# Kernel optimization log

Measured on AMD Instinct MI355X. Metric: run time of the kernel, lower is better.

Reference implementation:

```python
import jax, jax.numpy as jnp
import numpy as np

B, N, D, H = 4, 4096, 1024, 16
HD = D // H  # head dim = 64


def setup_inputs() -> dict:
    key = jax.random.key(0)
    k1, k2, k3 = jax.random.split(key, 3)
    x = jax.random.normal(k1, (B, N, D), dtype=jnp.float32)
    Wqkv = jax.random.normal(k2, (3 * D, D), dtype=jnp.float32) * (1.0 / np.sqrt(D))
    Wo = jax.random.normal(k3, (D, D), dtype=jnp.float32) * (1.0 / np.sqrt(D))
    bo = jnp.zeros((D,), dtype=jnp.float32)
    return {"x": x, "Wqkv": Wqkv, "Wo": Wo, "bo": bo}


def reference(x, Wqkv, Wo, bo):
    # qkv projection (no bias): [B,N,3D] -> [B,N,3,H,HD]
    qkv = jnp.einsum('bnd,ed->bne', x, Wqkv).reshape(B, N, 3, H, HD)
    q, k, v = qkv[:, :, 0], qkv[:, :, 1], qkv[:, :, 2]  # each [B,N,H,HD]
    # NOTE: faithful to source — heads are NOT moved to a batch axis, so
    # scores are [B,N,H,H]: attention mixes across heads per token.
    scores = jnp.einsum('bnhd,bngd->bnhg', q, k) / jnp.sqrt(jnp.float32(D))
    w = jax.nn.softmax(scores, axis=-1)            # [B,N,H,H]
    attn = jnp.einsum('bnhg,bngd->bnhd', w, v)     # [B,N,H,HD]
    attn = attn.reshape(B, N, D)
    return jnp.einsum('bnd,ed->bne', attn, Wo) + bo
```

## Files before the change

### kernel.cpp

```cpp
#include <hip/hip_runtime.h>
#include <hip/hip_bf16.h>

using bf16 = __hip_bfloat16;
typedef __attribute__((ext_vector_type(8))) short bf16x8;
typedef __attribute__((ext_vector_type(4))) float f32x4;

#define GLL(gp, lp) __builtin_amdgcn_global_load_lds( \
    (const __attribute__((address_space(1))) void*)(gp), \
    (__attribute__((address_space(3))) void*)(lp), 16, 0, 0)

#define BAR()    asm volatile("s_barrier" ::: "memory")
#define WAITV4() asm volatile("s_waitcnt vmcnt(4)" ::: "memory")
#define WAITV6() asm volatile("s_waitcnt vmcnt(6)" ::: "memory")
#define WAITV0() asm volatile("s_waitcnt vmcnt(0)" ::: "memory")
#define WAITL0() do { asm volatile("s_waitcnt lgkmcnt(0)" ::: "memory"); \
                      __builtin_amdgcn_sched_barrier(0); } while (0)
#define LHINT8() asm volatile("s_waitcnt lgkmcnt(8)" ::: "memory")

__device__ inline short bfbits(float f) {
  union { bf16 h; short s; } u;
  u.h = __float2bfloat16(f);
  return u.s;
}

__device__ inline bf16x8 ldcvt(const float* __restrict__ g) {
  const float4 f0 = *(const float4*)(g);
  const float4 f1 = *(const float4*)(g + 4);
  union { short s[8]; bf16x8 v; } u;
  u.s[0] = bfbits(f0.x); u.s[1] = bfbits(f0.y); u.s[2] = bfbits(f0.z); u.s[3] = bfbits(f0.w);
  u.s[4] = bfbits(f1.x); u.s[5] = bfbits(f1.y); u.s[6] = bfbits(f1.z); u.s[7] = bfbits(f1.w);
  return u.v;
}

__global__ __launch_bounds__(256)
void f32_to_bf16(const float* __restrict__ src, bf16* __restrict__ dst, int n8) {
  const int i = blockIdx.x * 256 + threadIdx.x;
  if (i < n8) *(bf16x8*)(dst + (size_t)i * 8) = ldcvt(src + (size_t)i * 8);
}

template <typename TC, bool SPLIT3>
__global__ __launch_bounds__(512)
void gemm256(const bf16* __restrict__ A, const bf16* __restrict__ B,
             const float* __restrict__ bias, TC* __restrict__ C,
             int K, int lda, int ldb, int ldc, int nbx) {
  __shared__ __align__(16) bf16 smem[4][256][64];
  const int tid  = threadIdx.x;
  const int lane = tid & 63;
  const int wave = tid >> 6;
  const int wm = wave >> 2;
  const int wn = wave & 3;

  int wg = blockIdx.x;
  const int nwg = gridDim.x;
  if ((nwg & 7) == 0) wg = (wg & 7) * (nwg >> 3) + (wg >> 3);
  const int m0 = (wg / nbx) * 256;
  const int n0 = (wg % nbx) * 256;

  const int srow = wave * 8 + (lane >> 3);
  const int scol = ((lane & 7) ^ (lane >> 3)) * 8;
  const bf16* gA = A + (size_t)(m0 + srow) * lda + scol;
  const bf16* gB = B + (size_t)(n0 + srow) * ldb + scol;

  const int fr = lane & 15, quad = lane >> 4, swz = fr & 7;

#define STAGE_A(buf, h, kt) do { \
    GLL(gA + (size_t)((h) * 128     ) * lda + (kt) * 64, &smem[buf][(h) * 128      + wave * 8][0]); \
    GLL(gA + (size_t)((h) * 128 + 64) * lda + (kt) * 64, &smem[buf][(h) * 128 + 64 + wave * 8][0]); \
  } while (0)
#define STAGE_B(buf, h, kt) do { \
    GLL(gB + (size_t)((h) * 128     ) * ldb + (kt) * 64, &smem[2 + (buf)][(h) * 128      + wave * 8][0]); \
    GLL(gB + (size_t)((h) * 128 + 64) * ldb + (kt) * 64, &smem[2 + (buf)][(h) * 128 + 64 + wave * 8][0]); \
  } while (0)
#define LDA_G(buf, mh) do { _Pragma("unroll") \
    for (int t = 0; t < 4; ++t) { _Pragma("unroll") \
      for (int ks = 0; ks < 2; ++ks) \
        av[t * 2 + ks] = *(const bf16x8*)&smem[buf][wm * 128 + (mh) * 64 + t * 16 + fr] \
                                             [(((ks << 2) | quad) ^ swz) << 3]; } } while (0)
#define LDB_G(buf, nh, dst) do { _Pragma("unroll") \
    for (int t = 0; t < 2; ++t) { _Pragma("unroll") \
      for (int ks = 0; ks < 2; ++ks) \
        dst[t * 2 + ks] = *(const bf16x8*)&smem[2 + (buf)][wn * 64 + (nh) * 32 + t * 16 + fr] \
                                              [(((ks << 2) | quad) ^ swz) << 3]; } } while (0)
#define MFMA_Q(mh, nh, bb) do { \
    __builtin_amdgcn_s_setprio(1); \
    _Pragma("unroll") \
    for (int t = 0; t < 4; ++t) { _Pragma("unroll") \
      for (int u = 0; u < 2; ++u) { _Pragma("unroll") \
        for (int ks = 0; ks < 2; ++ks) \
          acc[(mh) * 4 + t][(nh) * 2 + u] = __builtin_amdgcn_mfma_f32_16x16x32_bf16( \
              av[t * 2 + ks], bb[u * 2 + ks], acc[(mh) * 4 + t][(nh) * 2 + u], 0, 0, 0); } } \
    __builtin_amdgcn_s_setprio(0); } while (0)

  bf16x8 av[8], b0[4], b1[4];
  f32x4 acc[8][4] = {};

  STAGE_A(0, 0, 0); STAGE_A(0, 1, 0);
  STAGE_B(0, 0, 0); STAGE_B(0, 1, 0);
  STAGE_B(1, 0, 1); STAGE_B(1, 1, 1);
  STAGE_A(1, 0, 1);
  WAITV6(); BAR();

  const int KT = K >> 6;
  const int NI = KT >> 1;
  for (int i = 0; i < NI; ++i) {
    const int kt1 = 2 * i + 1;
    const int ka  = (2 * i + 2 < KT) ? 2 * i + 2 : 0;
    const int kb  = (2 * i + 3 < KT) ? 2 * i + 3 : 0;

    LDA_G(0, 0); LDB_G(0, 0, b0); STAGE_A(1, 1, kt1);
    LHINT8();
    BAR(); WAITL0(); MFMA_Q(0, 0, b0); BAR();
    LDB_G(0, 1, b1);
    BAR(); WAITL0(); MFMA_Q(0, 1, b1); BAR();
    LDA_G(0, 1); STAGE_B(0, 0, ka);
    BAR(); WAITL0(); MFMA_Q(1, 1, b1); BAR();
    STAGE_B(0, 1, ka); WAITV4();
    BAR(); WAITL0(); MFMA_Q(1, 0, b0); BAR();
    LDA_G(1, 0); LDB_G(1, 0, b0); STAGE_A(0, 0, ka);
    LHINT8();
    BAR(); WAITL0(); MFMA_Q(0, 0, b0); BAR();
    LDB_G(1, 1, b1); STAGE_A(0, 1, ka);
    BAR(); WAITL0(); MFMA_Q(0, 1, b1); BAR();
    LDA_G(1, 1); STAGE_B(1, 0, kb);
    BAR(); WAITL0(); MFMA_Q(1, 1, b1); BAR();
    STAGE_B(1, 1, kb); STAGE_A(1, 0, kb); WAITV6();
    BAR(); WAITL0(); MFMA_Q(1, 0, b0); BAR();
  }
  WAITV0(); BAR();

  const int rq = quad * 4;
  char* myc = (char*)(&smem[0][0][0]) + wave * 16384;
  float bvv[4];
#pragma unroll
  for (int nj = 0; nj < 4; ++nj)
    bvv[nj] = bias ? bias[n0 + wn * 64 + nj * 16 + fr] : 0.0f;

  const int cn0 = n0 + wn * 64;

  if constexpr (sizeof(TC) == 2) {
#pragma unroll
    for (int mi = 0; mi < 8; ++mi)
#pragma unroll
      for (int nj = 0; nj < 4; ++nj)
#pragma unroll
        for (int r = 0; r < 4; ++r) {
          const int row   = mi * 16 + rq + r;
          const int chunk = ((nj << 1) | (fr >> 3)) ^ (row & 7);
          *(short*)(myc + row * 128 + chunk * 16 + (fr & 7) * 2) =
              bfbits(acc[mi][nj][r] + bvv[nj]);
        }
    asm volatile("s_waitcnt lgkmcnt(0)" ::: "memory");
    __builtin_amdgcn_sched_barrier(0);
    const int rr = lane >> 3, rc = (lane & 7) ^ (lane >> 3);
    size_t cbase;
    if constexpr (SPLIT3)
      cbase = ((size_t)(cn0 >> 10) << 24) + (size_t)(m0 + wm * 128) * 1024 + (cn0 & 1023);
    else
      cbase = (size_t)(m0 + wm * 128) * ldc + cn0;
    const int cstride = SPLIT3 ? 1024 : ldc;
#pragma unroll
    for (int j = 0; j < 16; ++j) {
      const int row = j * 8 + rr;
      const uint4 d = *(const uint4*)(myc + row * 128 + rc * 16);
      *(uint4*)((bf16*)C + cbase + (size_t)row * cstride + (lane & 7) * 8) = d;
    }
  } else {
#pragma unroll
    for (int p = 0; p < 2; ++p) {
#pragma unroll
      for (int mi = 0; mi < 4; ++mi)
#pragma unroll
        for (int nj = 0; nj < 4; ++nj)
#pragma unroll
          for (int r = 0; r < 4; ++r) {
            const int row   = mi * 16 + rq + r;
            const int col   = nj * 16 + fr;
            const int chunk = (col >> 2) ^ (row & 7);
            *(float*)(myc + row * 256 + chunk * 16 + (col & 3) * 4) =
                acc[p * 4 + mi][nj][r] + bvv[nj];
          }
      asm volatile("s_waitcnt lgkmcnt(0)" ::: "memory");
      __builtin_amdgcn_sched_barrier(0);
      const int rr = lane >> 4, rc0 = lane & 15;
#pragma unroll
      for (int j = 0; j < 16; ++j) {
        const int row   = j * 4 + rr;
        const int chunk = rc0 ^ (row & 7);
        const uint4 d = *(const uint4*)(myc + row * 256 + chunk * 16);
        *(uint4*)((float*)C + (size_t)(m0 + wm * 128 + p * 64 + row) * ldc
                  + cn0 + rc0 * 4) = d;
      }
      if (p == 0) {
        asm volatile("s_waitcnt lgkmcnt(0)" ::: "memory");
        __builtin_amdgcn_sched_barrier(0);
      }
    }
  }
#undef STAGE_A
#undef STAGE_B
#undef LDA_G
#undef LDB_G
#undef MFMA_Q
}

__global__ __launch_bounds__(256)
void attn_heads(bf16* __restrict__ qp, const bf16* __restrict__ kp,
                const bf16* __restrict__ vp) {
  __shared__ __align__(16) bf16  s_qkv[4][3072];
  __shared__ __align__(16) float s_w[4][256];
  const int lane = threadIdx.x & 63;
  const int wave = threadIdx.x >> 6;
  const size_t tok = (size_t)blockIdx.x * 4 + wave;
  bf16*       qrow = qp + tok * 1024;
  const bf16* krow = kp + tok * 1024;
  const bf16* vrow = vp + tok * 1024;

#pragma unroll
  for (int i = 0; i < 2; ++i) {
    const int off = (i * 64 + lane) * 8;
    *(uint4*)(&s_qkv[wave][off])        = *(const uint4*)(qrow + off);
    *(uint4*)(&s_qkv[wave][1024 + off]) = *(const uint4*)(krow + off);
    *(uint4*)(&s_qkv[wave][2048 + off]) = *(const uint4*)(vrow + off);
  }
  __syncthreads();

  const bf16* sq = s_qkv[wave];
  const int fr   = lane & 15;
  const int quad = lane >> 4;

  f32x4 sc = {0.f, 0.f, 0.f, 0.f};
#pragma unroll
  for (int c = 0; c < 2; ++c) {
    bf16x8 a = *(const bf16x8*)&sq[fr * 64 + c * 32 + quad * 8];
    bf16x8 b = *(const bf16x8*)&sq[1024 + fr * 64 + c * 32 + quad * 8];
    sc = __builtin_amdgcn_mfma_f32_16x16x32_bf16(a, b, sc, 0, 0, 0);
  }

#pragma unroll
  for (int r = 0; r < 4; ++r) {
    float s = sc[r] * 0.03125f;
    float mx = s;
#pragma unroll
    for (int msk = 1; msk < 16; msk <<= 1) mx = fmaxf(mx, __shfl_xor(mx, msk, 64));
    float e = __expf(s - mx);
    float sum = e;
#pragma unroll
    for (int msk = 1; msk < 16; msk <<= 1) sum += __shfl_xor(sum, msk, 64);
    s_w[wave][(quad * 4 + r) * 16 + fr] = e / sum;
  }
  __syncthreads();

  float vv[16];
#pragma unroll
  for (int g = 0; g < 16; ++g) vv[g] = __bfloat162float(sq[2048 + g * 64 + lane]);
  const float* wrow = s_w[wave];
#pragma unroll
  for (int h = 0; h < 16; ++h) {
    float o = 0.f;
#pragma unroll
    for (int g4 = 0; g4 < 4; ++g4) {
      f32x4 w4 = *(const f32x4*)&wrow[h * 16 + g4 * 4];
      o += w4.x * vv[g4 * 4 + 0] + w4.y * vv[g4 * 4 + 1] +
           w4.z * vv[g4 * 4 + 2] + w4.w * vv[g4 * 4 + 3];
    }
    qrow[h * 64 + lane] = __float2bfloat16(o);
  }
}

extern "C" void kernel_launch(void* const* d_in, const int* in_sizes, int n_in,
                              void* d_out, int out_size, void* d_ws, size_t ws_size,
                              hipStream_t stream) {
  const float* x    = (const float*)d_in[0];
  const float* Wqkv = (const float*)d_in[1];
  const float* Wo   = (const float*)d_in[2];
  const float* bo   = (const float*)d_in[3];

  bf16* qp = (bf16*)d_ws;
  bf16* kp = qp + ((size_t)1 << 24);
  bf16* vp = qp + ((size_t)2 << 24);

  bf16* xb    = (bf16*)d_out;
  bf16* wqkvb = xb + 16777216;

  f32_to_bf16<<<8192, 256, 0, stream>>>(x, xb, 2097152);
  f32_to_bf16<<<1536, 256, 0, stream>>>(Wqkv, wqkvb, 393216);

  gemm256<bf16, true><<<768, 512, 0, stream>>>(
      xb, wqkvb, nullptr, qp, 1024, 1024, 1024, 1024, 12);

  attn_heads<<<4096, 256, 0, stream>>>(qp, kp, vp);

  f32_to_bf16<<<512, 256, 0, stream>>>(Wo, vp, 131072);

  gemm256<float, false><<<256, 512, 0, stream>>>(
      qp, vp, bo, (float*)d_out, 1024, 1024, 1024, 1024, 4);
}
```

Before: 288.7 us.

## Rewrite GEMM main loop with 32x32x16 MFMA and k-slice register double-buffering

Replaces the 16x16x32 MFMA quadrant schedule with 32x32x16 MFMAs and a new pipeline. The pipeline stages full 256-row A/B tiles per k-tile into two LDS buffers and double-buffers per-k-slice fragments in registers, waiting on partial lgkmcnt. Barriers are reduced to roughly two per k-tile instead of two per MFMA quadrant, and launch bounds now request two waves per SIMD. The epilogue is rewritten for the 32x32 accumulator layout. This aims to cut LDS read traffic and barrier stalls, at the risk of a shallower global prefetch (WAITV0 each tile) and extra register pressure.

```diff
diff --git a/kernel.cpp b/kernel.cpp
--- a/kernel.cpp
+++ b/kernel.cpp
@@ -4,18 +4,18 @@
 using bf16 = __hip_bfloat16;
 typedef __attribute__((ext_vector_type(8))) short bf16x8;
 typedef __attribute__((ext_vector_type(4))) float f32x4;
+typedef __attribute__((ext_vector_type(16))) float f32x16;
 
 #define GLL(gp, lp) __builtin_amdgcn_global_load_lds( \
     (const __attribute__((address_space(1))) void*)(gp), \
     (__attribute__((address_space(3))) void*)(lp), 16, 0, 0)
 
 #define BAR()    asm volatile("s_barrier" ::: "memory")
-#define WAITV4() asm volatile("s_waitcnt vmcnt(4)" ::: "memory")
-#define WAITV6() asm volatile("s_waitcnt vmcnt(6)" ::: "memory")
 #define WAITV0() asm volatile("s_waitcnt vmcnt(0)" ::: "memory")
-#define WAITL0() do { asm volatile("s_waitcnt lgkmcnt(0)" ::: "memory"); \
+#define LGKM6()  do { asm volatile("s_waitcnt lgkmcnt(6)" ::: "memory"); \
                       __builtin_amdgcn_sched_barrier(0); } while (0)
-#define LHINT8() asm volatile("s_waitcnt lgkmcnt(8)" ::: "memory")
+#define LGKM0()  do { asm volatile("s_waitcnt lgkmcnt(0)" ::: "memory"); \
+                      __builtin_amdgcn_sched_barrier(0); } while (0)
 
 __device__ inline short bfbits(float f) {
   union { bf16 h; short s; } u;
@@ -39,11 +39,12 @@
 }
 
 template <typename TC, bool SPLIT3>
-__global__ __launch_bounds__(512)
+__global__ __launch_bounds__(512, 2)
 void gemm256(const bf16* __restrict__ A, const bf16* __restrict__ B,
              const float* __restrict__ bias, TC* __restrict__ C,
              int K, int lda, int ldb, int ldc, int nbx) {
   __shared__ __align__(16) bf16 smem[4][256][64];
+  char* lds = (char*)&smem[0][0][0];
   const int tid  = threadIdx.x;
   const int lane = tid & 63;
   const int wave = tid >> 6;
@@ -61,96 +62,95 @@
   const bf16* gA = A + (size_t)(m0 + srow) * lda + scol;
   const bf16* gB = B + (size_t)(n0 + srow) * ldb + scol;
 
-  const int fr = lane & 15, quad = lane >> 4, swz = fr & 7;
-
-#define STAGE_A(buf, h, kt) do { \
-    GLL(gA + (size_t)((h) * 128     ) * lda + (kt) * 64, &smem[buf][(h) * 128      + wave * 8][0]); \
-    GLL(gA + (size_t)((h) * 128 + 64) * lda + (kt) * 64, &smem[buf][(h) * 128 + 64 + wave * 8][0]); \
+  const int r32 = lane & 31, h = lane >> 5, swz = r32 & 7;
+  int aad[4], bad[4];
+#pragma unroll
+  for (int ks = 0; ks < 4; ++ks) {
+    const int ck = (((2 * ks + h) ^ swz) << 4);
+    aad[ks] = ((wm * 128 + r32) << 7) + ck;
+    bad[ks] = ((wn * 64 + r32) << 7) + 65536 + ck;
+  }
+
+#define STAGE_A(buf, kt) do { \
+    GLL(gA + (size_t)(  0) * lda + (kt) * 64, lds + (buf) * 32768 + ((  0 + wave * 8) << 7)); \
+    GLL(gA + (size_t)( 64) * lda + (kt) * 64, lds + (buf) * 32768 + (( 64 + wave * 8) << 7)); \
+    GLL(gA + (size_t)(128) * lda + (kt) * 64, lds + (buf) * 32768 + ((128 + wave * 8) << 7)); \
+    GLL(gA + (size_t)(192) * lda + (kt) * 64, lds + (buf) * 32768 + ((192 + wave * 8) << 7)); \
   } while (0)
-#define STAGE_B(buf, h, kt) do { \
-    GLL(gB + (size_t)((h) * 128     ) * ldb + (kt) * 64, &smem[2 + (buf)][(h) * 128      + wave * 8][0]); \
-    GLL(gB + (size_t)((h) * 128 + 64) * ldb + (kt) * 64, &smem[2 + (buf)][(h) * 128 + 64 + wave * 8][0]); \
+#define STAGE_B(buf, kt) do { \
+    GLL(gB + (size_t)(  0) * ldb + (kt) * 64, lds + 65536 + (buf) * 32768 + ((  0 + wave * 8) << 7)); \
+    GLL(gB + (size_t)( 64) * ldb + (kt) * 64, lds + 65536 + (buf) * 32768 + (( 64 + wave * 8) << 7)); \
+    GLL(gB + (size_t)(128) * ldb + (kt) * 64, lds + 65536 + (buf) * 32768 + ((128 + wave * 8) << 7)); \
+    GLL(gB + (size_t)(192) * ldb + (kt) * 64, lds + 65536 + (buf) * 32768 + ((192 + wave * 8) << 7)); \
   } while (0)
-#define LDA_G(buf, mh) do { _Pragma("unroll") \
-    for (int t = 0; t < 4; ++t) { _Pragma("unroll") \
-      for (int ks = 0; ks < 2; ++ks) \
-        av[t * 2 + ks] = *(const bf16x8*)&smem[buf][wm * 128 + (mh) * 64 + t * 16 + fr] \
-                                             [(((ks << 2) | quad) ^ swz) << 3]; } } while (0)
-#define LDB_G(buf, nh, dst) do { _Pragma("unroll") \
-    for (int t = 0; t < 2; ++t) { _Pragma("unroll") \
-      for (int ks = 0; ks < 2; ++ks) \
-        dst[t * 2 + ks] = *(const bf16x8*)&smem[2 + (buf)][wn * 64 + (nh) * 32 + t * 16 + fr] \
-                                              [(((ks << 2) | quad) ^ swz) << 3]; } } while (0)
-#define MFMA_Q(mh, nh, bb) do { \
+#define LD6(afX, bfX, buf, ks) do { \
+    afX[0] = *(const bf16x8*)(lds + aad[ks] + ((buf) * 32768 +     0)); \
+    afX[1] = *(const bf16x8*)(lds + aad[ks] + ((buf) * 32768 +  4096)); \
+    afX[2] = *(const bf16x8*)(lds + aad[ks] + ((buf) * 32768 +  8192)); \
+    afX[3] = *(const bf16x8*)(lds + aad[ks] + ((buf) * 32768 + 12288)); \
+    bfX[0] = *(const bf16x8*)(lds + bad[ks] + ((buf) * 32768 +     0)); \
+    bfX[1] = *(const bf16x8*)(lds + bad[ks] + ((buf) * 32768 +  4096)); \
+  } while (0)
+#define MFMA8(afX, bfX) do { \
     __builtin_amdgcn_s_setprio(1); \
     _Pragma("unroll") \
-    for (int t = 0; t < 4; ++t) { _Pragma("unroll") \
-      for (int u = 0; u < 2; ++u) { _Pragma("unroll") \
-        for (int ks = 0; ks < 2; ++ks) \
-          acc[(mh) * 4 + t][(nh) * 2 + u] = __builtin_amdgcn_mfma_f32_16x16x32_bf16( \
-              av[t * 2 + ks], bb[u * 2 + ks], acc[(mh) * 4 + t][(nh) * 2 + u], 0, 0, 0); } } \
+    for (int m = 0; m < 4; ++m) { _Pragma("unroll") \
+      for (int n = 0; n < 2; ++n) \
+        acc[m][n] = __builtin_amdgcn_mfma_f32_32x32x16_bf16( \
+            afX[m], bfX[n], acc[m][n], 0, 0, 0); } \
     __builtin_amdgcn_s_setprio(0); } while (0)
 
-  bf16x8 av[8], b0[4], b1[4];
-  f32x4 acc[8][4] = {};
-
-  STAGE_A(0, 0, 0); STAGE_A(0, 1, 0);
-  STAGE_B(0, 0, 0); STAGE_B(0, 1, 0);
-  STAGE_B(1, 0, 1); STAGE_B(1, 1, 1);
-  STAGE_A(1, 0, 1);
-  WAITV6(); BAR();
+  f32x16 acc[4][2] = {};
+  bf16x8 af0[4], af1[4], bf0[2], bf1[2];
+
+  STAGE_A(0, 0); STAGE_B(0, 0);
+  WAITV0(); BAR();
+  LD6(af0, bf0, 0, 0);
 
   const int KT = K >> 6;
   const int NI = KT >> 1;
   for (int i = 0; i < NI; ++i) {
     const int kt1 = 2 * i + 1;
     const int ka  = (2 * i + 2 < KT) ? 2 * i + 2 : 0;
-    const int kb  = (2 * i + 3 < KT) ? 2 * i + 3 : 0;
-
-    LDA_G(0, 0); LDB_G(0, 0, b0); STAGE_A(1, 1, kt1);
-    LHINT8();
-    BAR(); WAITL0(); MFMA_Q(0, 0, b0); BAR();
-    LDB_G(0, 1, b1);
-    BAR(); WAITL0(); MFMA_Q(0, 1, b1); BAR();
-    LDA_G(0, 1); STAGE_B(0, 0, ka);
-    BAR(); WAITL0(); MFMA_Q(1, 1, b1); BAR();
-    STAGE_B(0, 1, ka); WAITV4();
-    BAR(); WAITL0(); MFMA_Q(1, 0, b0); BAR();
-    LDA_G(1, 0); LDB_G(1, 0, b0); STAGE_A(0, 0, ka);
-    LHINT8();
-    BAR(); WAITL0(); MFMA_Q(0, 0, b0); BAR();
-    LDB_G(1, 1, b1); STAGE_A(0, 1, ka);
-    BAR(); WAITL0(); MFMA_Q(0, 1, b1); BAR();
-    LDA_G(1, 1); STAGE_B(1, 0, kb);
-    BAR(); WAITL0(); MFMA_Q(1, 1, b1); BAR();
-    STAGE_B(1, 1, kb); STAGE_A(1, 0, kb); WAITV6();
-    BAR(); WAITL0(); MFMA_Q(1, 0, b0); BAR();
-  }
-  WAITV0(); BAR();
-
-  const int rq = quad * 4;
-  char* myc = (char*)(&smem[0][0][0]) + wave * 16384;
-  float bvv[4];
-#pragma unroll
-  for (int nj = 0; nj < 4; ++nj)
-    bvv[nj] = bias ? bias[n0 + wn * 64 + nj * 16 + fr] : 0.0f;
+    LD6(af1, bf1, 0, 1); STAGE_A(1, kt1); STAGE_B(1, kt1);
+    LGKM6(); MFMA8(af0, bf0);
+    LD6(af0, bf0, 0, 2);
+    LGKM6(); MFMA8(af1, bf1);
+    LD6(af1, bf1, 0, 3);
+    WAITV0(); LGKM6(); MFMA8(af0, bf0); BAR();
+    LD6(af0, bf0, 1, 0);
+    LGKM6(); MFMA8(af1, bf1); BAR();
+    LD6(af1, bf1, 1, 1); STAGE_A(0, ka); STAGE_B(0, ka);
+    LGKM6(); MFMA8(af0, bf0);
+    LD6(af0, bf0, 1, 2);
+    LGKM6(); MFMA8(af1, bf1);
+    LD6(af1, bf1, 1, 3);
+    WAITV0(); LGKM6(); MFMA8(af0, bf0); BAR();
+    LD6(af0, bf0, 0, 0);
+    LGKM6(); MFMA8(af1, bf1); BAR();
+  }
+  WAITV0(); LGKM0(); BAR();
 
   const int cn0 = n0 + wn * 64;
+  float bvv[2];
+  bvv[0] = bias ? bias[cn0 + r32] : 0.0f;
+  bvv[1] = bias ? bias[cn0 + 32 + r32] : 0.0f;
+  char* myc = lds + wave * 16384;
 
   if constexpr (sizeof(TC) == 2) {
 #pragma unroll
-    for (int mi = 0; mi < 8; ++mi)
-#pragma unroll
-      for (int nj = 0; nj < 4; ++nj)
-#pragma unroll
-        for (int r = 0; r < 4; ++r) {
-          const int row   = mi * 16 + rq + r;
-          const int chunk = ((nj << 1) | (fr >> 3)) ^ (row & 7);
-          *(short*)(myc + row * 128 + chunk * 16 + (fr & 7) * 2) =
-              bfbits(acc[mi][nj][r] + bvv[nj]);
+    for (int m = 0; m < 4; ++m)
+#pragma unroll
+      for (int n = 0; n < 2; ++n)
+#pragma unroll
+        for (int r = 0; r < 16; ++r) {
+          const int row = m * 32 + (r & 3) + ((r >> 2) << 3) + (h << 2);
+          const int col = (n << 5) + r32;
+          const int chunk = (col >> 3) ^ (row & 7);
+          *(short*)(myc + row * 128 + (chunk << 4) + ((col & 7) << 1)) =
+              bfbits(acc[m][n][r] + bvv[n]);
         }
-    asm volatile("s_waitcnt lgkmcnt(0)" ::: "memory");
-    __builtin_amdgcn_sched_barrier(0);
+    LGKM0();
     const int rr = lane >> 3, rc = (lane & 7) ^ (lane >> 3);
     size_t cbase;
     if constexpr (SPLIT3)
@@ -168,39 +168,34 @@
 #pragma unroll
     for (int p = 0; p < 2; ++p) {
 #pragma unroll
-      for (int mi = 0; mi < 4; ++mi)
-#pragma unroll
-        for (int nj = 0; nj < 4; ++nj)
-#pragma unroll
-          for (int r = 0; r < 4; ++r) {
-            const int row   = mi * 16 + rq + r;
-            const int col   = nj * 16 + fr;
+      for (int mm = 0; mm < 2; ++mm)
+#pragma unroll
+        for (int n = 0; n < 2; ++n)
+#pragma unroll
+          for (int r = 0; r < 16; ++r) {
+            const int row = mm * 32 + (r & 3) + ((r >> 2) << 3) + (h << 2);
+            const int col = (n << 5) + r32;
             const int chunk = (col >> 2) ^ (row & 7);
-            *(float*)(myc + row * 256 + chunk * 16 + (col & 3) * 4) =
-                acc[p * 4 + mi][nj][r] + bvv[nj];
+            *(float*)(myc + row * 256 + (chunk << 4) + ((col & 3) << 2)) =
+                acc[p * 2 + mm][n][r] + bvv[n];
           }
-      asm volatile("s_waitcnt lgkmcnt(0)" ::: "memory");
-      __builtin_amdgcn_sched_barrier(0);
+      LGKM0();
       const int rr = lane >> 4, rc0 = lane & 15;
 #pragma unroll
       for (int j = 0; j < 16; ++j) {
-        const int row   = j * 4 + rr;
+        const int row = j * 4 + rr;
         const int chunk = rc0 ^ (row & 7);
         const uint4 d = *(const uint4*)(myc + row * 256 + chunk * 16);
         *(uint4*)((float*)C + (size_t)(m0 + wm * 128 + p * 64 + row) * ldc
                   + cn0 + rc0 * 4) = d;
       }
-      if (p == 0) {
-        asm volatile("s_waitcnt lgkmcnt(0)" ::: "memory");
-        __builtin_amdgcn_sched_barrier(0);
-      }
+      if (p == 0) LGKM0();
     }
   }
 #undef STAGE_A
 #undef STAGE_B
-#undef LDA_G
-#undef LDB_G
-#undef MFMA_Q
+#undef LD6
+#undef MFMA8
 }
 
 __global__ __launch_bounds__(256)
@@ -255,15 +250,15 @@
   for (int g = 0; g < 16; ++g) vv[g] = __bfloat162float(sq[2048 + g * 64 + lane]);
   const float* wrow = s_w[wave];
 #pragma unroll
-  for (int h = 0; h < 16; ++h) {
+  for (int hh = 0; hh < 16; ++hh) {
     float o = 0.f;
 #pragma unroll
     for (int g4 = 0; g4 < 4; ++g4) {
-      f32x4 w4 = *(const f32x4*)&wrow[h * 16 + g4 * 4];
+      f32x4 w4 = *(const f32x4*)&wrow[hh * 16 + g4 * 4];
       o += w4.x * vv[g4 * 4 + 0] + w4.y * vv[g4 * 4 + 1] +
            w4.z * vv[g4 * 4 + 2] + w4.w * vv[g4 * 4 + 3];
     }
-    qrow[h * 64 + lane] = __float2bfloat16(o);
+    qrow[hh * 64 + lane] = __float2bfloat16(o);
   }
 }
 
```

Measured after the change: 304.0 us. +5.3%, slower.

## Replace output projection GEMM with smaller 128x128 tile kernel

Applied to the files above, without the earlier changes.

Adds a new 128x128-tile, 256-thread NT GEMM kernel with single-buffered LDS staging, and uses it for the final output projection in place of the 256x256 pipelined kernel. The grid grows from 256 to 1024 workgroups, which may improve occupancy and load balance across CUs. In exchange the new kernel drops the multi-stage prefetch pipeline, syncs twice per 32-wide K step and writes its fp32 output with scattered scalar stores, so per-tile efficiency is likely lower.

```diff
diff --git a/kernel.cpp b/kernel.cpp
--- a/kernel.cpp
+++ b/kernel.cpp
@@ -32,10 +32,91 @@
   return u.v;
 }
 
+__device__ inline void store_c(float* C, size_t idx, float v) { C[idx] = v; }
+__device__ inline void store_c(bf16*  C, size_t idx, float v) { C[idx] = __float2bfloat16(v); }
+
 __global__ __launch_bounds__(256)
 void f32_to_bf16(const float* __restrict__ src, bf16* __restrict__ dst, int n8) {
   const int i = blockIdx.x * 256 + threadIdx.x;
   if (i < n8) *(bf16x8*)(dst + (size_t)i * 8) = ldcvt(src + (size_t)i * 8);
+}
+
+template <typename TB, typename TC>
+__global__ __launch_bounds__(256)
+void gemm_nt(const bf16* __restrict__ A, const TB* __restrict__ B,
+             const float* __restrict__ bias, TC* __restrict__ C,
+             int K, int lda, int ldb, int ldc) {
+  constexpr bool B_F32 = sizeof(TB) == 4;
+  __shared__ __align__(16) bf16 As[128 * 32];
+  __shared__ __align__(16) bf16 Bs[128 * 32];
+  const int tid  = threadIdx.x;
+  const int lane = tid & 63;
+  const int wave = tid >> 6;
+  const int wm = wave >> 1, wn = wave & 1;
+  const int m0 = blockIdx.y * 128;
+  const int n0 = blockIdx.x * 128;
+
+  const int srow = wave * 16 + (lane >> 2);
+  const int scol = (lane & 3) * 8;
+  const bf16* gA0 = A + (size_t)(m0 + srow) * lda + scol;
+  const bf16* gA1 = A + (size_t)(m0 + 64 + srow) * lda + scol;
+  const TB*   gB0 = B + (size_t)(n0 + srow) * ldb + scol;
+  const TB*   gB1 = B + (size_t)(n0 + 64 + srow) * ldb + scol;
+  bf16* lA0 = &As[(wave * 16) * 32];
+  bf16* lA1 = lA0 + 64 * 32;
+  bf16* lB0u = &Bs[(wave * 16) * 32];
+  bf16* lB1u = lB0u + 64 * 32;
+  bf16* lB0p = &Bs[srow * 32 + scol];
+  bf16* lB1p = lB0p + 64 * 32;
+
+  const int fr = lane & 15;
+  const int kq = (lane >> 4) * 8;
+  f32x4 acc[4][4] = {};
+
+  for (int k0 = 0; k0 < K; k0 += 32) {
+    bf16x8 b0, b1;
+    if constexpr (B_F32) {
+      b0 = ldcvt((const float*)gB0 + k0);
+      b1 = ldcvt((const float*)gB1 + k0);
+    }
+    __syncthreads();
+    GLL(gA0 + k0, lA0);
+    GLL(gA1 + k0, lA1);
+    if constexpr (B_F32) {
+      *(bf16x8*)lB0p = b0;
+      *(bf16x8*)lB1p = b1;
+    } else {
+      GLL((const bf16*)gB0 + k0, lB0u);
+      GLL((const bf16*)gB1 + k0, lB1u);
+    }
+    __syncthreads();
+    bf16x8 af[4], bfv[4];
+#pragma unroll
+    for (int t = 0; t < 4; ++t) {
+      af[t]  = *(const bf16x8*)&As[(wm * 64 + t * 16 + fr) * 32 + kq];
+      bfv[t] = *(const bf16x8*)&Bs[(wn * 64 + t * 16 + fr) * 32 + kq];
+    }
+#pragma unroll
+    for (int i = 0; i < 4; ++i)
+#pragma unroll
+      for (int j = 0; j < 4; ++j)
+        acc[i][j] = __builtin_amdgcn_mfma_f32_16x16x32_bf16(af[i], bfv[j], acc[i][j], 0, 0, 0);
+  }
+
+  const int rq  = (lane >> 4) * 4;
+  const int col = lane & 15;
+#pragma unroll
+  for (int j = 0; j < 4; ++j) {
+    const int cn = n0 + wn * 64 + j * 16 + col;
+    const float bv = bias ? bias[cn] : 0.0f;
+#pragma unroll
+    for (int i = 0; i < 4; ++i) {
+      const int cm = m0 + wm * 64 + i * 16 + rq;
+#pragma unroll
+      for (int r = 0; r < 4; ++r)
+        store_c(C, (size_t)(cm + r) * ldc + cn, acc[i][j][r] + bv);
+    }
+  }
 }
 
 template <typename TC, bool SPLIT3>
@@ -255,15 +336,15 @@
   for (int g = 0; g < 16; ++g) vv[g] = __bfloat162float(sq[2048 + g * 64 + lane]);
   const float* wrow = s_w[wave];
 #pragma unroll
-  for (int h = 0; h < 16; ++h) {
+  for (int hh = 0; hh < 16; ++hh) {
     float o = 0.f;
 #pragma unroll
     for (int g4 = 0; g4 < 4; ++g4) {
-      f32x4 w4 = *(const f32x4*)&wrow[h * 16 + g4 * 4];
+      f32x4 w4 = *(const f32x4*)&wrow[hh * 16 + g4 * 4];
       o += w4.x * vv[g4 * 4 + 0] + w4.y * vv[g4 * 4 + 1] +
            w4.z * vv[g4 * 4 + 2] + w4.w * vv[g4 * 4 + 3];
     }
-    qrow[h * 64 + lane] = __float2bfloat16(o);
+    qrow[hh * 64 + lane] = __float2bfloat16(o);
   }
 }
 
@@ -292,6 +373,6 @@
 
   f32_to_bf16<<<512, 256, 0, stream>>>(Wo, vp, 131072);
 
-  gemm256<float, false><<<256, 512, 0, stream>>>(
-      qp, vp, bo, (float*)d_out, 1024, 1024, 1024, 1024, 4);
-}
+  gemm_nt<bf16, float><<<dim3(8, 128), 256, 0, stream>>>(
+      qp, vp, bo, (float*)d_out, 1024, 1024, 1024, 1024);
+}
```

Result: slower. 317.5 us (+10.0%).
